# Optimization experiments

Hardware: AMD Instinct MI355X
Metric: run time of the kernel (lower is better)

## Reference

```python
import jax, jax.numpy as jnp
import numpy as np
from jax import lax

INPUT_DIM = 784
HIDDEN_DIM = 512
BATCH = 1024


def setup_inputs() -> dict:
    key = jax.random.key(0)
    k_x, k_inw, k_hw = jax.random.split(key, 3)
    # binarized inputs (values >= 0, so the Bernoulli sampling branch in the
    # original torch.where(x_i < 0, ...) is never taken -> deterministic fwd)
    x = (jax.random.uniform(k_x, (BATCH, INPUT_DIM)) > 0.5).astype(jnp.float32)
    # kaiming_normal_ fan_in init as in the torch module
    in_W = jax.random.normal(k_inw, (HIDDEN_DIM, INPUT_DIM), jnp.float32) * np.sqrt(2.0 / INPUT_DIM)
    in_b = jnp.zeros((HIDDEN_DIM,), jnp.float32)
    h_W = jax.random.normal(k_hw, (INPUT_DIM, HIDDEN_DIM), jnp.float32) * np.sqrt(2.0 / HIDDEN_DIM)
    h_b = jnp.zeros((INPUT_DIM,), jnp.float32)
    return {"x": x, "in_W": in_W, "in_b": in_b, "h_W": h_W, "h_b": h_b}


def reference(x, in_W, in_b, h_W, h_b):
    # x: [B, D]; in_W: [H, D]; in_b: [H]; h_W: [D, H]; h_b: [D]
    B = x.shape[0]
    a0 = jnp.zeros((B, in_b.shape[0]), x.dtype) + in_b  # a = in_b expanded over batch

    def step(a, inp):
        w_col, hw_row, hb_i, x_i = inp  # [H], [H], [], [B]
        h = jax.nn.relu(a)                              # [B, H]
        p_i = jax.nn.sigmoid(h @ hw_row + hb_i)         # [B]
        a_new = a + x_i[:, None] * w_col[None, :]       # rank-1 update
        return a_new, p_i

    _, p = lax.scan(step, a0, (in_W.T, h_W, h_b, x.T))  # p: [D, B]
    return p.T  # p_hat: [B, D]
```

## Files before the change

### kernel.cpp

```cpp
#include <hip/hip_runtime.h>

#define D_IN    784
#define HDIM    512
#define BATCH_N 1024
#define TCH     8
#define NCH     (D_IN / TCH)
#define CHW     (TCH * HDIM)

__device__ __forceinline__ float relu_(float v) { return fmaxf(v, 0.0f); }

__global__ __launch_bounds__(256, 1)
void transpose_inW(const float* __restrict__ inW, float* __restrict__ wT) {
    int idx = blockIdx.x * 256 + threadIdx.x;
    if (idx < D_IN * HDIM) {
        int i = idx / HDIM;
        int h = idx - i * HDIM;
        wT[idx] = inW[(size_t)h * D_IN + i];
    }
}

__device__ __forceinline__ void load8(float (&d)[8], const float* p) {
    float4 v0 = *(const float4*)(p);
    float4 v1 = *(const float4*)(p + 4);
    d[0]=v0.x; d[1]=v0.y; d[2]=v0.z; d[3]=v0.w;
    d[4]=v1.x; d[5]=v1.y; d[6]=v1.z; d[7]=v1.w;
}

__device__ __forceinline__ void stage_chunk(const float* __restrict__ hW,
                                            const float* __restrict__ wT,
                                            float* dhw, float* dwt,
                                            int i0, int w, int l) {
    const float* src = (w < 2) ? (hW + (size_t)i0 * HDIM + w * 2048)
                               : (wT + (size_t)i0 * HDIM + (w - 2) * 2048);
    float* dst = (w < 2) ? (dhw + w * 2048) : (dwt + (w - 2) * 2048);
    #pragma unroll
    for (int j = 0; j < 8; ++j) {
        __builtin_amdgcn_global_load_lds(
            (const __attribute__((address_space(1))) void*)(src + j * 256 + l * 4),
            (__attribute__((address_space(3))) void*)(dst + j * 256 + l * 4),
            16, 0, 0);
    }
}

__device__ __forceinline__ void compute_chunk(const float* __restrict__ bhw,
                                              const float* __restrict__ bwt,
                                              const float (&xs)[8],
                                              const float (&hb)[8],
                                              float (&a)[8],
                                              float* __restrict__ sp,
                                              float* __restrict__ orow,
                                              int i0, int l) {
    float part[TCH];
    #pragma unroll
    for (int t = 0; t < TCH; ++t) {
        const float* hp = bhw + t * HDIM;
        float4 hw0 = *(const float4*)(hp + 4 * l);
        float4 hw1 = *(const float4*)(hp + 256 + 4 * l);
        float init = (l == 0) ? hb[t] : 0.0f;
        float p0 = fmaf(relu_(a[0]), hw0.x, init);
        p0 = fmaf(relu_(a[1]), hw0.y, p0);
        p0 = fmaf(relu_(a[2]), hw0.z, p0);
        p0 = fmaf(relu_(a[3]), hw0.w, p0);
        float p1 = relu_(a[4]) * hw1.x;
        p1 = fmaf(relu_(a[5]), hw1.y, p1);
        p1 = fmaf(relu_(a[6]), hw1.z, p1);
        p1 = fmaf(relu_(a[7]), hw1.w, p1);
        part[t] = p0 + p1;

        const float* wp = bwt + t * HDIM;
        float4 w0 = *(const float4*)(wp + 4 * l);
        float4 w1 = *(const float4*)(wp + 256 + 4 * l);
        const float xi = xs[t];
        a[0] = fmaf(xi, w0.x, a[0]); a[1] = fmaf(xi, w0.y, a[1]);
        a[2] = fmaf(xi, w0.z, a[2]); a[3] = fmaf(xi, w0.w, a[3]);
        a[4] = fmaf(xi, w1.x, a[4]); a[5] = fmaf(xi, w1.y, a[5]);
        a[6] = fmaf(xi, w1.z, a[6]); a[7] = fmaf(xi, w1.w, a[7]);
    }

    #pragma unroll
    for (int t = 0; t < TCH; ++t) sp[t * 64 + l] = part[t];

    const int t = l >> 3;
    const int c = l & 7;
    const float* pr = sp + t * 64 + c * 8;
    float4 q0 = *(const float4*)(pr);
    float4 q1 = *(const float4*)(pr + 4);
    float v = ((q0.x + q0.y) + (q0.z + q0.w)) + ((q1.x + q1.y) + (q1.z + q1.w));
    v += __shfl_xor(v, 1, 64);
    v += __shfl_xor(v, 2, 64);
    v += __shfl_xor(v, 4, 64);
    float r = __builtin_amdgcn_rcpf(1.0f + __expf(-v));
    if ((l & 7) == 0) orow[i0 + t] = r;
}

__global__ __launch_bounds__(256, 1)
void nade_fwd2(const float* __restrict__ x,
               const float* __restrict__ in_b,
               const float* __restrict__ hW,
               const float* __restrict__ h_b,
               const float* __restrict__ wT,
               float* __restrict__ out) {
    __shared__ float s_hw[2][CHW];
    __shared__ float s_wt[2][CHW];
    __shared__ float s_p[4 * 512];

    const int tid = threadIdx.x;
    const int w = tid >> 6;
    const int l = tid & 63;
    const int row = blockIdx.x * 4 + w;

    float a[8];
    {
        float4 b0 = *(const float4*)(in_b + 4 * l);
        float4 b1 = *(const float4*)(in_b + 256 + 4 * l);
        a[0]=b0.x; a[1]=b0.y; a[2]=b0.z; a[3]=b0.w;
        a[4]=b1.x; a[5]=b1.y; a[6]=b1.z; a[7]=b1.w;
    }

    const float* xrow = x + (size_t)row * D_IN;
    float* orow = out + (size_t)row * D_IN;
    float* sp = s_p + w * 512;

    float xsA[8], xsB[8], hbA[8], hbB[8];
    load8(xsA, xrow);
    load8(hbA, h_b);

    stage_chunk(hW, wT, s_hw[0], s_wt[0], 0, w, l);
    __syncthreads();

    for (int cc = 0; cc < NCH / 2; ++cc) {
        const int c = 2 * cc;

        stage_chunk(hW, wT, s_hw[1], s_wt[1], (c + 1) * TCH, w, l);
        load8(xsB, xrow + (c + 1) * TCH);
        load8(hbB, h_b + (c + 1) * TCH);
        compute_chunk(s_hw[0], s_wt[0], xsA, hbA, a, sp, orow, c * TCH, l);
        __syncthreads();

        if (c + 2 < NCH) {
            stage_chunk(hW, wT, s_hw[0], s_wt[0], (c + 2) * TCH, w, l);
            load8(xsA, xrow + (c + 2) * TCH);
            load8(hbA, h_b + (c + 2) * TCH);
        }
        compute_chunk(s_hw[1], s_wt[1], xsB, hbB, a, sp, orow, (c + 1) * TCH, l);
        __syncthreads();
    }
}

__global__ __launch_bounds__(64, 1)
void nade_fwd_fallback(const float* __restrict__ x,
                       const float* __restrict__ in_W,
                       const float* __restrict__ in_b,
                       const float* __restrict__ hW,
                       const float* __restrict__ h_b,
                       float* __restrict__ out) {
    const int b  = blockIdx.x;
    const int l  = threadIdx.x;
    const int h0 = l * 8;

    float a[8];
    {
        float4 b0 = *(const float4*)(in_b + h0);
        float4 b1 = *(const float4*)(in_b + h0 + 4);
        a[0]=b0.x; a[1]=b0.y; a[2]=b0.z; a[3]=b0.w;
        a[4]=b1.x; a[5]=b1.y; a[6]=b1.z; a[7]=b1.w;
    }
    const float* xrow = x + (size_t)b * D_IN;
    float* orow = out + (size_t)b * D_IN;

    for (int i = 0; i < D_IN; ++i) {
        const float4 hw0 = *(const float4*)(hW + (size_t)i * HDIM + h0);
        const float4 hw1 = *(const float4*)(hW + (size_t)i * HDIM + h0 + 4);
        float p;
        p = relu_(a[0]) * hw0.x;
        p = fmaf(relu_(a[1]), hw0.y, p);
        p = fmaf(relu_(a[2]), hw0.z, p);
        p = fmaf(relu_(a[3]), hw0.w, p);
        p = fmaf(relu_(a[4]), hw1.x, p);
        p = fmaf(relu_(a[5]), hw1.y, p);
        p = fmaf(relu_(a[6]), hw1.z, p);
        p = fmaf(relu_(a[7]), hw1.w, p);
        #pragma unroll
        for (int s = 1; s < 64; s <<= 1) p += __shfl_xor(p, s, 64);
        if (l == 0) orow[i] = 1.0f / (1.0f + __expf(-(p + h_b[i])));

        const float xi = xrow[i];
        if (xi != 0.0f) {
            a[0] = fmaf(xi, in_W[(size_t)(h0+0)*D_IN + i], a[0]);
            a[1] = fmaf(xi, in_W[(size_t)(h0+1)*D_IN + i], a[1]);
            a[2] = fmaf(xi, in_W[(size_t)(h0+2)*D_IN + i], a[2]);
            a[3] = fmaf(xi, in_W[(size_t)(h0+3)*D_IN + i], a[3]);
            a[4] = fmaf(xi, in_W[(size_t)(h0+4)*D_IN + i], a[4]);
            a[5] = fmaf(xi, in_W[(size_t)(h0+5)*D_IN + i], a[5]);
            a[6] = fmaf(xi, in_W[(size_t)(h0+6)*D_IN + i], a[6]);
            a[7] = fmaf(xi, in_W[(size_t)(h0+7)*D_IN + i], a[7]);
        }
    }
}

extern "C" void kernel_launch(void* const* d_in, const int* in_sizes, int n_in,
                              void* d_out, int out_size, void* d_ws, size_t ws_size,
                              hipStream_t stream) {
    const float* x    = (const float*)d_in[0];
    const float* in_W = (const float*)d_in[1];
    const float* in_b = (const float*)d_in[2];
    const float* hW   = (const float*)d_in[3];
    const float* h_b  = (const float*)d_in[4];
    float* out = (float*)d_out;

    const size_t need = (size_t)D_IN * HDIM * sizeof(float);
    if (ws_size >= need) {
        float* wT = (float*)d_ws;
        hipLaunchKernelGGL(transpose_inW,
                           dim3((D_IN * HDIM + 255) / 256), dim3(256), 0, stream,
                           in_W, wT);
        hipLaunchKernelGGL(nade_fwd2,
                           dim3(BATCH_N / 4), dim3(256), 0, stream,
                           x, in_b, hW, h_b, wT, out);
    } else {
        hipLaunchKernelGGL(nade_fwd_fallback,
                           dim3(BATCH_N), dim3(64), 0, stream,
                           x, in_W, in_b, hW, h_b, out);
    }
}
```

Baseline: 133.4 us.

## Split sequential scan into segments with precomputed checkpoint activations

Splits the 784-step recurrence into 7 segments. Each segment's starting activation is precomputed by a segment-sum GEMM-like kernel followed by a prefix kernel over segments, so the main kernel can process all segments in parallel across a 2D grid with 8 rows per block. This removes the long serial dependency that left only 256 blocks each walking all 784 steps. In exchange it needs a large checkpoint workspace (7×1024×512 floats), adds two extra launches and extra global traffic, and falls back to the slow path if the workspace is too small.

```diff
diff --git a/kernel.cpp b/kernel.cpp
--- a/kernel.cpp
+++ b/kernel.cpp
@@ -3,11 +3,20 @@
 #define D_IN    784
 #define HDIM    512
 #define BATCH_N 1024
-#define TCH     8
-#define NCH     (D_IN / TCH)
-#define CHW     (TCH * HDIM)
+
+#define NSEG    7
+#define SEGLEN  112
+#define TC      4
+#define NCH2    (SEGLEN / TC)
+
+#define WT_FLOATS   ((size_t)D_IN * HDIM)
+#define CKPT_STRIDE ((size_t)BATCH_N * HDIM)
+#define CKPT_FLOATS ((size_t)NSEG * CKPT_STRIDE)
 
 __device__ __forceinline__ float relu_(float v) { return fmaxf(v, 0.0f); }
+__device__ __forceinline__ float sigmoid_(float v) {
+    return __builtin_amdgcn_rcpf(1.0f + __expf(-v));
+}
 
 __global__ __launch_bounds__(256, 1)
 void transpose_inW(const float* __restrict__ inW, float* __restrict__ wT) {
@@ -19,132 +28,168 @@
     }
 }
 
-__device__ __forceinline__ void load8(float (&d)[8], const float* p) {
-    float4 v0 = *(const float4*)(p);
-    float4 v1 = *(const float4*)(p + 4);
-    d[0]=v0.x; d[1]=v0.y; d[2]=v0.z; d[3]=v0.w;
-    d[4]=v1.x; d[5]=v1.y; d[6]=v1.z; d[7]=v1.w;
-}
-
-__device__ __forceinline__ void stage_chunk(const float* __restrict__ hW,
-                                            const float* __restrict__ wT,
-                                            float* dhw, float* dwt,
-                                            int i0, int w, int l) {
-    const float* src = (w < 2) ? (hW + (size_t)i0 * HDIM + w * 2048)
-                               : (wT + (size_t)i0 * HDIM + (w - 2) * 2048);
-    float* dst = (w < 2) ? (dhw + w * 2048) : (dwt + (w - 2) * 2048);
+__global__ __launch_bounds__(256, 4)
+void seg_sums(const float* __restrict__ x, const float* __restrict__ wT,
+              float* __restrict__ ckpt) {
+    const int rt = blockIdx.x;
+    const int k  = blockIdx.y;
+    const int tid = threadIdx.x;
+    const int r2 = tid >> 5;
+    const int hc = tid & 31;
+    const int r0 = rt * 16 + r2;
+    const int r1 = r0 + 8;
+    const int i0 = k * SEGLEN;
+
+    float acc0[16], acc1[16];
     #pragma unroll
-    for (int j = 0; j < 8; ++j) {
-        __builtin_amdgcn_global_load_lds(
-            (const __attribute__((address_space(1))) void*)(src + j * 256 + l * 4),
-            (__attribute__((address_space(3))) void*)(dst + j * 256 + l * 4),
-            16, 0, 0);
-    }
-}
-
-__device__ __forceinline__ void compute_chunk(const float* __restrict__ bhw,
-                                              const float* __restrict__ bwt,
-                                              const float (&xs)[8],
-                                              const float (&hb)[8],
-                                              float (&a)[8],
-                                              float* __restrict__ sp,
-                                              float* __restrict__ orow,
-                                              int i0, int l) {
-    float part[TCH];
+    for (int j = 0; j < 16; ++j) { acc0[j] = 0.0f; acc1[j] = 0.0f; }
+
+    const float* x0 = x + (size_t)r0 * D_IN + i0;
+    const float* x1 = x + (size_t)r1 * D_IN + i0;
+    const float* w  = wT + (size_t)i0 * HDIM + hc * 4;
+
+    for (int i = 0; i < SEGLEN; ++i) {
+        const float xa = x0[i];
+        const float xb = x1[i];
+        const float* wr = w + (size_t)i * HDIM;
+        #pragma unroll
+        for (int j = 0; j < 4; ++j) {
+            float4 wv = *(const float4*)(wr + j * 128);
+            acc0[4*j+0] = fmaf(xa, wv.x, acc0[4*j+0]);
+            acc0[4*j+1] = fmaf(xa, wv.y, acc0[4*j+1]);
+            acc0[4*j+2] = fmaf(xa, wv.z, acc0[4*j+2]);
+            acc0[4*j+3] = fmaf(xa, wv.w, acc0[4*j+3]);
+            acc1[4*j+0] = fmaf(xb, wv.x, acc1[4*j+0]);
+            acc1[4*j+1] = fmaf(xb, wv.y, acc1[4*j+1]);
+            acc1[4*j+2] = fmaf(xb, wv.z, acc1[4*j+2]);
+            acc1[4*j+3] = fmaf(xb, wv.w, acc1[4*j+3]);
+        }
+    }
+
+    float* g0 = ckpt + (size_t)(k + 1) * CKPT_STRIDE + (size_t)r0 * HDIM + hc * 4;
+    float* g1 = ckpt + (size_t)(k + 1) * CKPT_STRIDE + (size_t)r1 * HDIM + hc * 4;
     #pragma unroll
-    for (int t = 0; t < TCH; ++t) {
-        const float* hp = bhw + t * HDIM;
-        float4 hw0 = *(const float4*)(hp + 4 * l);
-        float4 hw1 = *(const float4*)(hp + 256 + 4 * l);
-        float init = (l == 0) ? hb[t] : 0.0f;
-        float p0 = fmaf(relu_(a[0]), hw0.x, init);
-        p0 = fmaf(relu_(a[1]), hw0.y, p0);
-        p0 = fmaf(relu_(a[2]), hw0.z, p0);
-        p0 = fmaf(relu_(a[3]), hw0.w, p0);
-        float p1 = relu_(a[4]) * hw1.x;
-        p1 = fmaf(relu_(a[5]), hw1.y, p1);
-        p1 = fmaf(relu_(a[6]), hw1.z, p1);
-        p1 = fmaf(relu_(a[7]), hw1.w, p1);
-        part[t] = p0 + p1;
-
-        const float* wp = bwt + t * HDIM;
-        float4 w0 = *(const float4*)(wp + 4 * l);
-        float4 w1 = *(const float4*)(wp + 256 + 4 * l);
-        const float xi = xs[t];
-        a[0] = fmaf(xi, w0.x, a[0]); a[1] = fmaf(xi, w0.y, a[1]);
-        a[2] = fmaf(xi, w0.z, a[2]); a[3] = fmaf(xi, w0.w, a[3]);
-        a[4] = fmaf(xi, w1.x, a[4]); a[5] = fmaf(xi, w1.y, a[5]);
-        a[6] = fmaf(xi, w1.z, a[6]); a[7] = fmaf(xi, w1.w, a[7]);
-    }
-
+    for (int j = 0; j < 4; ++j) {
+        *(float4*)(g0 + j * 128) = make_float4(acc0[4*j+0], acc0[4*j+1], acc0[4*j+2], acc0[4*j+3]);
+        *(float4*)(g1 + j * 128) = make_float4(acc1[4*j+0], acc1[4*j+1], acc1[4*j+2], acc1[4*j+3]);
+    }
+}
+
+__global__ __launch_bounds__(256, 4)
+void prefix_ck(const float* __restrict__ in_b, float* __restrict__ ckpt) {
+    int idx = blockIdx.x * 256 + threadIdx.x;
+    int b  = idx >> 7;
+    int hq = idx & 127;
+    float* p = ckpt + (size_t)b * HDIM + hq * 4;
+    float4 cur = *(const float4*)(in_b + hq * 4);
+    *(float4*)p = cur;
     #pragma unroll
-    for (int t = 0; t < TCH; ++t) sp[t * 64 + l] = part[t];
-
-    const int t = l >> 3;
-    const int c = l & 7;
-    const float* pr = sp + t * 64 + c * 8;
-    float4 q0 = *(const float4*)(pr);
-    float4 q1 = *(const float4*)(pr + 4);
-    float v = ((q0.x + q0.y) + (q0.z + q0.w)) + ((q1.x + q1.y) + (q1.z + q1.w));
-    v += __shfl_xor(v, 1, 64);
-    v += __shfl_xor(v, 2, 64);
-    v += __shfl_xor(v, 4, 64);
-    float r = __builtin_amdgcn_rcpf(1.0f + __expf(-v));
-    if ((l & 7) == 0) orow[i0 + t] = r;
-}
-
-__global__ __launch_bounds__(256, 1)
-void nade_fwd2(const float* __restrict__ x,
-               const float* __restrict__ in_b,
+    for (int k = 1; k < NSEG; ++k) {
+        float4 g = *(const float4*)(p + k * CKPT_STRIDE);
+        cur.x += g.x; cur.y += g.y; cur.z += g.z; cur.w += g.w;
+        *(float4*)(p + k * CKPT_STRIDE) = cur;
+    }
+}
+
+__global__ __launch_bounds__(512, 6)
+void nade_fwd3(const float* __restrict__ x,
+               const float* __restrict__ ckpt,
                const float* __restrict__ hW,
                const float* __restrict__ h_b,
                const float* __restrict__ wT,
                float* __restrict__ out) {
-    __shared__ float s_hw[2][CHW];
-    __shared__ float s_wt[2][CHW];
-    __shared__ float s_p[4 * 512];
+    __shared__ float sbuf[2][2 * TC * HDIM];
 
     const int tid = threadIdx.x;
-    const int w = tid >> 6;
-    const int l = tid & 63;
-    const int row = blockIdx.x * 4 + w;
+    const int w   = tid >> 6;
+    const int l   = tid & 63;
+    const int row = blockIdx.x * 8 + w;
+    const int k   = blockIdx.y;
+    const int base = k * SEGLEN;
 
     float a[8];
     {
-        float4 b0 = *(const float4*)(in_b + 4 * l);
-        float4 b1 = *(const float4*)(in_b + 256 + 4 * l);
-        a[0]=b0.x; a[1]=b0.y; a[2]=b0.z; a[3]=b0.w;
-        a[4]=b1.x; a[5]=b1.y; a[6]=b1.z; a[7]=b1.w;
-    }
-
-    const float* xrow = x + (size_t)row * D_IN;
-    float* orow = out + (size_t)row * D_IN;
-    float* sp = s_p + w * 512;
-
-    float xsA[8], xsB[8], hbA[8], hbB[8];
-    load8(xsA, xrow);
-    load8(hbA, h_b);
-
-    stage_chunk(hW, wT, s_hw[0], s_wt[0], 0, w, l);
+        const float* ap = ckpt + (size_t)k * CKPT_STRIDE + (size_t)row * HDIM;
+        float4 a0 = *(const float4*)(ap + 4 * l);
+        float4 a1 = *(const float4*)(ap + 256 + 4 * l);
+        a[0]=a0.x; a[1]=a0.y; a[2]=a0.z; a[3]=a0.w;
+        a[4]=a1.x; a[5]=a1.y; a[6]=a1.z; a[7]=a1.w;
+    }
+
+    const float* xrow = x   + (size_t)row * D_IN + base;
+    float*       orow = out + (size_t)row * D_IN + base;
+    const float* hbp  = h_b + base;
+
+#define STAGE(buf_, c_) {                                                        \
+        const int i0_ = base + (c_) * TC;                                        \
+        const float* src_ = (w < 4) ? (hW + (size_t)i0_ * HDIM + w * 512)        \
+                                    : (wT + (size_t)i0_ * HDIM + (w - 4) * 512); \
+        float* dst_ = &sbuf[buf_][w * 512];                                      \
+        __builtin_amdgcn_global_load_lds(                                        \
+            (const __attribute__((address_space(1))) void*)(src_ + l * 4),       \
+            (__attribute__((address_space(3))) void*)(dst_ + l * 4), 16, 0, 0);  \
+        __builtin_amdgcn_global_load_lds(                                        \
+            (const __attribute__((address_space(1))) void*)(src_ + 256 + l * 4), \
+            (__attribute__((address_space(3))) void*)(dst_ + 256 + l * 4), 16, 0, 0); \
+    }
+
+    STAGE(0, 0);
     __syncthreads();
 
-    for (int cc = 0; cc < NCH / 2; ++cc) {
-        const int c = 2 * cc;
-
-        stage_chunk(hW, wT, s_hw[1], s_wt[1], (c + 1) * TCH, w, l);
-        load8(xsB, xrow + (c + 1) * TCH);
-        load8(hbB, h_b + (c + 1) * TCH);
-        compute_chunk(s_hw[0], s_wt[0], xsA, hbA, a, sp, orow, c * TCH, l);
+    for (int c = 0; c < NCH2; ++c) {
+        const int buf = c & 1;
+        if (c + 1 < NCH2) STAGE(buf ^ 1, c + 1);
+
+        const float* bh = &sbuf[buf][0];
+        const float* bw = &sbuf[buf][2048];
+
+        float4 xv  = *(const float4*)(xrow + c * TC);
+        float4 hbv = *(const float4*)(hbp  + c * TC);
+        const float xs[4] = {xv.x, xv.y, xv.z, xv.w};
+        const float hb[4] = {hbv.x, hbv.y, hbv.z, hbv.w};
+
+        float part[4];
+        #pragma unroll
+        for (int t = 0; t < TC; ++t) {
+            const float* hp = bh + t * HDIM;
+            float4 h0 = *(const float4*)(hp + 4 * l);
+            float4 h1 = *(const float4*)(hp + 256 + 4 * l);
+            float init = (l == 0) ? hb[t] : 0.0f;
+            float p0 = fmaf(relu_(a[0]), h0.x, init);
+            p0 = fmaf(relu_(a[1]), h0.y, p0);
+            p0 = fmaf(relu_(a[2]), h0.z, p0);
+            p0 = fmaf(relu_(a[3]), h0.w, p0);
+            float p1 = relu_(a[4]) * h1.x;
+            p1 = fmaf(relu_(a[5]), h1.y, p1);
+            p1 = fmaf(relu_(a[6]), h1.z, p1);
+            p1 = fmaf(relu_(a[7]), h1.w, p1);
+            part[t] = p0 + p1;
+
+            const float* wp = bw + t * HDIM;
+            float4 w0 = *(const float4*)(wp + 4 * l);
+            float4 w1 = *(const float4*)(wp + 256 + 4 * l);
+            const float xi = xs[t];
+            a[0] = fmaf(xi, w0.x, a[0]); a[1] = fmaf(xi, w0.y, a[1]);
+            a[2] = fmaf(xi, w0.z, a[2]); a[3] = fmaf(xi, w0.w, a[3]);
+            a[4] = fmaf(xi, w1.x, a[4]); a[5] = fmaf(xi, w1.y, a[5]);
+            a[6] = fmaf(xi, w1.z, a[6]); a[7] = fmaf(xi, w1.w, a[7]);
+        }
+
+        #pragma unroll
+        for (int s = 1; s < 64; s <<= 1) {
+            #pragma unroll
+            for (int t = 0; t < TC; ++t)
+                part[t] += __shfl_xor(part[t], s, 64);
+        }
+
+        if (l == 0) {
+            float4 rv = make_float4(sigmoid_(part[0]), sigmoid_(part[1]),
+                                    sigmoid_(part[2]), sigmoid_(part[3]));
+            *(float4*)(orow + c * TC) = rv;
+        }
         __syncthreads();
-
-        if (c + 2 < NCH) {
-            stage_chunk(hW, wT, s_hw[0], s_wt[0], (c + 2) * TCH, w, l);
-            load8(xsA, xrow + (c + 2) * TCH);
-            load8(hbA, h_b + (c + 2) * TCH);
-        }
-        compute_chunk(s_hw[1], s_wt[1], xsB, hbB, a, sp, orow, (c + 1) * TCH, l);
-        __syncthreads();
-    }
+    }
+#undef STAGE
 }
 
 __global__ __launch_bounds__(64, 1)
@@ -182,7 +227,7 @@
         p = fmaf(relu_(a[7]), hw1.w, p);
         #pragma unroll
         for (int s = 1; s < 64; s <<= 1) p += __shfl_xor(p, s, 64);
-        if (l == 0) orow[i] = 1.0f / (1.0f + __expf(-(p + h_b[i])));
+        if (l == 0) orow[i] = sigmoid_(p + h_b[i]);
 
         const float xi = xrow[i];
         if (xi != 0.0f) {
@@ -208,15 +253,24 @@
     const float* h_b  = (const float*)d_in[4];
     float* out = (float*)d_out;
 
-    const size_t need = (size_t)D_IN * HDIM * sizeof(float);
-    if (ws_size >= need) {
-        float* wT = (float*)d_ws;
+    const size_t need_full = (WT_FLOATS + CKPT_FLOATS) * sizeof(float);
+
+    if (ws_size >= need_full) {
+        float* wT   = (float*)d_ws;
+        float* ckpt = wT + WT_FLOATS;
+
         hipLaunchKernelGGL(transpose_inW,
                            dim3((D_IN * HDIM + 255) / 256), dim3(256), 0, stream,
                            in_W, wT);
-        hipLaunchKernelGGL(nade_fwd2,
-                           dim3(BATCH_N / 4), dim3(256), 0, stream,
-                           x, in_b, hW, h_b, wT, out);
+        hipLaunchKernelGGL(seg_sums,
+                           dim3(BATCH_N / 16, NSEG - 1), dim3(256), 0, stream,
+                           x, wT, ckpt);
+        hipLaunchKernelGGL(prefix_ck,
+                           dim3(BATCH_N * (HDIM / 4) / 256), dim3(256), 0, stream,
+                           in_b, ckpt);
+        hipLaunchKernelGGL(nade_fwd3,
+                           dim3(BATCH_N / 8, NSEG), dim3(512), 0, stream,
+                           x, ckpt, hW, h_b, wT, out);
     } else {
         hipLaunchKernelGGL(nade_fwd_fallback,
                            dim3(BATCH_N), dim3(64), 0, stream,
```

Result: slower. 220.3 us (+65.2%).
